# Performance work log

Hardware: AMD Instinct MI355X
Metric: run time of the kernel (lower is better)

Reference implementation:

```python
import jax, jax.numpy as jnp
import numpy as np

D_H, D_G, D_PROJ = 1280, 768, 256
SCALE = D_PROJ ** (-0.5)

def setup_inputs() -> dict:
    key = jax.random.key(0)
    k1, k2, k3, k4 = jax.random.split(key, 4)
    B, L, T = 8, 4096, 512
    H = jax.random.normal(k1, (B, L, D_H), dtype=jnp.float32)
    G = jax.random.normal(k2, (B, T, D_G), dtype=jnp.float32)
    attn_mask = jnp.zeros((B, L), dtype=bool)  # True = pad/ignore
    # nn.Linear weights: (out_features, in_features)
    Wk = jax.random.normal(k3, (D_PROJ, D_H), dtype=jnp.float32) * (D_H ** -0.5)
    Wq = jax.random.normal(k4, (D_PROJ, D_G), dtype=jnp.float32) * (D_G ** -0.5)
    return {"H": H, "G": G, "attn_mask": attn_mask, "Wk": Wk, "Wq": Wq}

def reference(H, G, attn_mask, Wk, Wq):
    # K = Wk(H): (B,L,P); Q = Wq(G): (B,T,P)
    K = jnp.einsum('bld,pd->blp', H, Wk)
    Q = jnp.einsum('btd,pd->btp', G, Wq)
    # scores (B,T,L); streaming two-pass softmax in the original is exactly
    # softmax over L -> compute it stably in one fused expression here.
    logits = jnp.einsum('btp,blp->btl', Q, K) * SCALE
    logits = jnp.where(attn_mask[:, None, :], -jnp.inf, logits)
    alpha = jax.nn.softmax(logits, axis=-1)
    Z = jnp.einsum('btl,bld->btd', alpha, H)  # (B,T,Dh)
    return Z
```

## Files before the change

kernel.cpp:

```cpp
#include <hip/hip_runtime.h>
#include <hip/hip_bf16.h>
#include <stdint.h>


typedef float f32x4 __attribute__((ext_vector_type(4)));
typedef short bf16x8 __attribute__((ext_vector_type(8)));

__device__ __forceinline__ unsigned short f2bf(float f) {
    __hip_bfloat16 h = __float2bfloat16(f);
    return __builtin_bit_cast(unsigned short, h);
}
__device__ __forceinline__ float bf2f(unsigned short h) {
    union { uint32_t u; float f; } v; v.u = ((uint32_t)h) << 16;
    return v.f;
}

__device__ __forceinline__ int xcdswz(int bx, int nbx) {
    int cpx = nbx >> 3;
    return (bx & 7) * cpx + (bx >> 3);
}

__device__ __forceinline__ void gload16(const unsigned short* g, unsigned short* l) {
    __builtin_amdgcn_global_load_lds(
        (const __attribute__((address_space(1))) void*)g,
        (__attribute__((address_space(3))) void*)l,
        16, 0, 0);
}

__device__ __forceinline__ int lidx(int row, int kshort) {
    return row * 40 + (((kshort >> 3) ^ ((row >> 3) & 3)) << 3) + (kshort & 7);
}

__global__ __launch_bounds__(256)
void cvt_f32_bf16(const float* __restrict__ in, unsigned short* __restrict__ out, long n4)
{
    long i = (long)blockIdx.x * 256 + threadIdx.x;
    if (i >= n4) return;
    float4 v = ((const float4*)in)[i];
    ushort4 w;
    w.x = f2bf(v.x); w.y = f2bf(v.y); w.z = f2bf(v.z); w.w = f2bf(v.w);
    ((ushort4*)out)[i] = w;
}

template<bool WRITE_HB>
__global__ __launch_bounds__(256)
void cvt_h(const float* __restrict__ H, unsigned short* __restrict__ Hbt,
           unsigned short* __restrict__ Hb)
{
    __shared__ unsigned short lT[64 * 72];
    const int ntile = 64 * 20 * 8;
    for (int tileid = blockIdx.x; tileid < ntile; tileid += gridDim.x) {
        int tmp = tileid;
        const int dt = tmp % 20; tmp /= 20;
        const int lt = tmp % 64;
        const int b  = tmp / 64;
        const int l0 = lt * 64, d0 = dt * 64;
        const float* Hs = H + ((long)b * 4096 + l0) * 1280 + d0;
        #pragma unroll
        for (int it = 0; it < 4; ++it) {
            int chunk = it * 256 + threadIdx.x;
            int lr = chunk >> 4, dc4 = (chunk & 15) << 2;
            float4 v = *(const float4*)(Hs + (long)lr * 1280 + dc4);
            unsigned short w[4] = { f2bf(v.x), f2bf(v.y), f2bf(v.z), f2bf(v.w) };
            if constexpr (WRITE_HB) {
                ushort4 wb = { w[0], w[1], w[2], w[3] };
                *(ushort4*)(Hb + ((long)b * 4096 + l0 + lr) * 1280 + d0 + dc4) = wb;
            }
            #pragma unroll
            for (int j = 0; j < 4; ++j) {
                int d = dc4 + j;
                int sl = (lr & 15) | ((((lr >> 4) ^ (d >> 2)) & 3) << 4);
                lT[d * 72 + sl] = w[j];
            }
        }
        __syncthreads();
        {
            int drow = threadIdx.x >> 2, lc = threadIdx.x & 3;
            int slc = lc ^ ((drow >> 2) & 3);
            const uint4* src = (const uint4*)(lT + drow * 72 + slc * 16);
            unsigned short* dst = Hbt + ((long)b * 1280 + d0 + drow) * 4096 + l0 + lc * 16;
            uint4 v0 = src[0], v1 = src[1];
            *(uint4*)(dst)     = v0;
            *(uint4*)(dst + 8) = v1;
        }
        __syncthreads();
    }
}

__global__ __launch_bounds__(256)
void gemm_proj(const float* __restrict__ Ap, const float* __restrict__ Bp,
               unsigned short* __restrict__ Cp, int M, int N, int K)
{
    __shared__ __align__(16) unsigned short lA[128 * 40];
    __shared__ __align__(16) unsigned short lB[128 * 40];

    const int bx = xcdswz(blockIdx.x, gridDim.x);
    const int nt = N >> 7;
    const int tm = bx / nt;
    const int tn = bx % nt;
    const int tid = threadIdx.x;
    const int lane = tid & 63, wv = tid >> 6;
    const int wr = wv >> 1, wc = wv & 1;
    const int fr = lane & 15, fk = lane >> 4;

    f32x4 acc[4][4] = {};

    for (int k0 = 0; k0 < K; k0 += 32) {
        {
            const float* A = Ap + (long)tm * 128 * K + k0;
            #pragma unroll
            for (int it = 0; it < 4; ++it) {
                int chunk = it * 256 + tid;
                int row = chunk >> 3;
                int kc  = (chunk & 7) << 2;
                const float4 v = *(const float4*)(A + (long)row * K + kc);
                ushort4 w;
                w.x = f2bf(v.x); w.y = f2bf(v.y); w.z = f2bf(v.z); w.w = f2bf(v.w);
                *(ushort4*)(&lA[lidx(row, kc)]) = w;
            }
        }
        {
            const float* B = Bp + (long)tn * 128 * K + k0;
            #pragma unroll
            for (int it = 0; it < 4; ++it) {
                int chunk = it * 256 + tid;
                int row = chunk >> 3;
                int kc  = (chunk & 7) << 2;
                const float4 v = *(const float4*)(B + (long)row * K + kc);
                ushort4 w;
                w.x = f2bf(v.x); w.y = f2bf(v.y); w.z = f2bf(v.z); w.w = f2bf(v.w);
                *(ushort4*)(&lB[lidx(row, kc)]) = w;
            }
        }
        __syncthreads();
        bf16x8 af[4], bfr[4];
        #pragma unroll
        for (int i = 0; i < 4; ++i)
            af[i] = *(const bf16x8*)(&lA[lidx(wr * 64 + i * 16 + fr, fk * 8)]);
        #pragma unroll
        for (int i = 0; i < 4; ++i)
            bfr[i] = *(const bf16x8*)(&lB[lidx(wc * 64 + i * 16 + fr, fk * 8)]);
        #pragma unroll
        for (int mi = 0; mi < 4; ++mi)
            #pragma unroll
            for (int ni = 0; ni < 4; ++ni)
                acc[mi][ni] = __builtin_amdgcn_mfma_f32_16x16x32_bf16(af[mi], bfr[ni], acc[mi][ni], 0, 0, 0);
        __syncthreads();
    }

    unsigned short* C = Cp + ((long)tm * 128) * N + (long)tn * 128;
    #pragma unroll
    for (int mi = 0; mi < 4; ++mi)
        #pragma unroll
        for (int ni = 0; ni < 4; ++ni)
            #pragma unroll
            for (int j = 0; j < 4; ++j) {
                int m = wr * 64 + mi * 16 + fk * 4 + j;
                int n = wc * 64 + ni * 16 + fr;
                C[(long)m * N + n] = f2bf(acc[mi][ni][j]);
            }
}

template<bool OF32>
__global__ __launch_bounds__(256)
void gemm_bt16s(const unsigned short* __restrict__ Ap, const unsigned short* __restrict__ Bp,
                void* __restrict__ Cp, int M, int N, int K,
                long sA, long sB, long sC, float scale)
{
    __shared__ __align__(16) unsigned short lA[128 * 64];
    __shared__ __align__(16) unsigned short lB[128 * 64];

    const int bx = xcdswz(blockIdx.x, gridDim.x);
    const int nt = N >> 7;
    const int tm = bx / nt, tn = bx % nt;
    const int b  = blockIdx.y;
    const int tid = threadIdx.x;
    const int lane = tid & 63, wv = tid >> 6;
    const int wr = wv >> 1, wc = wv & 1;
    const int fr = lane & 15, fk = lane >> 4;

    f32x4 acc[4][4] = {};

    const unsigned short* A0 = Ap + (long)b * sA + (long)tm * 128 * K;
    const unsigned short* B0 = Bp + (long)b * sB + (long)tn * 128 * K;

    for (int k0 = 0; k0 < K; k0 += 64) {
        #pragma unroll
        for (int q = 0; q < 4; ++q) {
            int slot = wv * 256 + q * 64 + lane;
            int row = slot >> 3, c = slot & 7;
            int ks = (c ^ (row & 7)) << 3;
            gload16(A0 + (long)row * K + k0 + ks, lA + (size_t)(wv * 256 + q * 64) * 8);
            gload16(B0 + (long)row * K + k0 + ks, lB + (size_t)(wv * 256 + q * 64) * 8);
        }
        __syncthreads();
        bf16x8 af[2][4], bfv[2][4];
        #pragma unroll
        for (int ks = 0; ks < 2; ++ks) {
            int csw = ((ks * 4 + fk) ^ (fr & 7)) << 3;
            #pragma unroll
            for (int i = 0; i < 4; ++i) {
                af[ks][i]  = *(const bf16x8*)(lA + (wr * 64 + i * 16 + fr) * 64 + csw);
                bfv[ks][i] = *(const bf16x8*)(lB + (wc * 64 + i * 16 + fr) * 64 + csw);
            }
        }
        #pragma unroll
        for (int mi = 0; mi < 4; ++mi)
            #pragma unroll
            for (int ni = 0; ni < 4; ++ni)
                #pragma unroll
                for (int ks = 0; ks < 2; ++ks)
                    acc[mi][ni] = __builtin_amdgcn_mfma_f32_16x16x32_bf16(af[ks][mi], bfv[ks][ni], acc[mi][ni], 0, 0, 0);
        __syncthreads();
    }

    if constexpr (OF32) {
        float* C = (float*)Cp + (long)b * sC + ((long)tm * 128) * N + (long)tn * 128;
        #pragma unroll
        for (int mi = 0; mi < 4; ++mi)
            #pragma unroll
            for (int ni = 0; ni < 4; ++ni)
                #pragma unroll
                for (int j = 0; j < 4; ++j) {
                    int m = wr * 64 + mi * 16 + fk * 4 + j;
                    int n = wc * 64 + ni * 16 + fr;
                    C[(long)m * N + n] = acc[mi][ni][j] * scale;
                }
    } else {
        unsigned short* C = (unsigned short*)Cp + (long)b * sC + ((long)tm * 128) * N + (long)tn * 128;
        #pragma unroll
        for (int mi = 0; mi < 4; ++mi)
            #pragma unroll
            for (int ni = 0; ni < 4; ++ni)
                #pragma unroll
                for (int j = 0; j < 4; ++j) {
                    int m = wr * 64 + mi * 16 + fk * 4 + j;
                    int n = wc * 64 + ni * 16 + fr;
                    C[(long)m * N + n] = f2bf(acc[mi][ni][j] * scale);
                }
    }
}

__global__ __launch_bounds__(256)
void gemm_kn(const unsigned short* __restrict__ Ap, const float* __restrict__ Bp,
             float* __restrict__ Cp, int M, int N, int K,
             long sA, long sB, long sC)
{
    __shared__ __align__(16) unsigned short lA[128 * 40];
    __shared__ __align__(16) unsigned short lB[64 * 40];

    const int bx = xcdswz(blockIdx.x, gridDim.x);
    const int mt = M >> 7;
    const int tm = bx % mt;
    const int tn = bx / mt;
    const int b  = blockIdx.y;
    const int tid = threadIdx.x;
    const int lane = tid & 63, wv = tid >> 6;
    const int wr = wv >> 1, wc = wv & 1;
    const int fr = lane & 15, fk = lane >> 4;

    f32x4 acc[4][2] = {};

    const unsigned short* A0 = Ap + (long)b * sA + (long)tm * 128 * K;
    const int nn    = tid & 63;
    const int khalf = tid >> 6;

    for (int k0 = 0; k0 < K; k0 += 32) {
        #pragma unroll
        for (int it = 0; it < 2; ++it) {
            int chunk = it * 256 + tid;
            int row = chunk >> 2;
            int kc  = (chunk & 3) << 3;
            *(uint4*)(&lA[lidx(row, kc)]) = *(const uint4*)(A0 + (long)row * K + k0 + kc);
        }
        {
            const float* Bb = Bp + (long)b * sB + (long)(k0 + khalf * 8) * N + (long)tn * 64 + nn;
            unsigned short t8[8];
            #pragma unroll
            for (int kk = 0; kk < 8; ++kk)
                t8[kk] = f2bf(Bb[(long)kk * N]);
            *(uint4*)(&lB[lidx(nn, khalf * 8)]) = *(uint4*)(&t8[0]);
        }
        __syncthreads();
        bf16x8 af[4], bfr[2];
        #pragma unroll
        for (int i = 0; i < 4; ++i)
            af[i] = *(const bf16x8*)(&lA[lidx(wr * 64 + i * 16 + fr, fk * 8)]);
        #pragma unroll
        for (int i = 0; i < 2; ++i)
            bfr[i] = *(const bf16x8*)(&lB[lidx(wc * 32 + i * 16 + fr, fk * 8)]);
        #pragma unroll
        for (int mi = 0; mi < 4; ++mi)
            #pragma unroll
            for (int ni = 0; ni < 2; ++ni)
                acc[mi][ni] = __builtin_amdgcn_mfma_f32_16x16x32_bf16(af[mi], bfr[ni], acc[mi][ni], 0, 0, 0);
        __syncthreads();
    }

    float* C = Cp + (long)b * sC + ((long)tm * 128) * N + (long)tn * 64;
    #pragma unroll
    for (int mi = 0; mi < 4; ++mi)
        #pragma unroll
        for (int ni = 0; ni < 2; ++ni)
            #pragma unroll
            for (int j = 0; j < 4; ++j) {
                int m = wr * 64 + mi * 16 + fk * 4 + j;
                int n = wc * 32 + ni * 16 + fr;
                C[(long)m * N + n] = acc[mi][ni][j];
            }
}

__global__ __launch_bounds__(256)
void softmax_rows(unsigned short* __restrict__ S, const unsigned char* __restrict__ mask)
{
    const int row = blockIdx.x;
    const int b = row >> 9;
    const long base = (long)row * 4096;
    const int tid = threadIdx.x, lane = tid & 63, wv = tid >> 6;
    __shared__ float red[8];

    uint4 s0 = *(const uint4*)(S + base + tid * 16);
    uint4 s1 = *(const uint4*)(S + base + tid * 16 + 8);
    uint4 mv = *(const uint4*)(mask + (long)b * 4096 + tid * 16);
    const unsigned char* mb = (const unsigned char*)&mv;

    unsigned int words[8] = { s0.x, s0.y, s0.z, s0.w, s1.x, s1.y, s1.z, s1.w };
    float x[16];
    #pragma unroll
    for (int i = 0; i < 8; ++i) {
        x[2 * i]     = bf2f((unsigned short)(words[i] & 0xffffu));
        x[2 * i + 1] = bf2f((unsigned short)(words[i] >> 16));
    }
    #pragma unroll
    for (int i = 0; i < 16; ++i)
        if (mb[i]) x[i] = -1e30f;

    float m = x[0];
    #pragma unroll
    for (int i = 1; i < 16; ++i) m = fmaxf(m, x[i]);
    #pragma unroll
    for (int off = 32; off; off >>= 1) m = fmaxf(m, __shfl_xor(m, off));
    if (lane == 0) red[wv] = m;
    __syncthreads();
    m = fmaxf(fmaxf(red[0], red[1]), fmaxf(red[2], red[3]));

    float p[16];
    float s = 0.f;
    #pragma unroll
    for (int i = 0; i < 16; ++i) { p[i] = __expf(x[i] - m); s += p[i]; }
    #pragma unroll
    for (int off = 32; off; off >>= 1) s += __shfl_xor(s, off);
    if (lane == 0) red[4 + wv] = s;
    __syncthreads();
    s = (red[4] + red[5]) + (red[6] + red[7]);
    const float inv = 1.0f / s;

    unsigned int ow[8];
    #pragma unroll
    for (int i = 0; i < 8; ++i) {
        unsigned int lo = f2bf(p[2 * i] * inv);
        unsigned int hi = f2bf(p[2 * i + 1] * inv);
        ow[i] = lo | (hi << 16);
    }
    uint4 o0 = { ow[0], ow[1], ow[2], ow[3] };
    uint4 o1 = { ow[4], ow[5], ow[6], ow[7] };
    *(uint4*)(S + base + tid * 16)     = o0;
    *(uint4*)(S + base + tid * 16 + 8) = o1;
}

extern "C" void kernel_launch(void* const* d_in, const int* in_sizes, int n_in,
                              void* d_out, int out_size, void* d_ws, size_t ws_size,
                              hipStream_t stream)
{
    const float*         H    = (const float*)d_in[0];
    const float*         G    = (const float*)d_in[1];
    const unsigned char* mask = (const unsigned char*)d_in[2];
    const float*         Wk   = (const float*)d_in[3];
    const float*         Wq   = (const float*)d_in[4];
    float*               out  = (float*)d_out;

    const long nK = (long)8 * 4096 * 256;
    const long nQ = (long)8 * 512 * 256;
    const long nS = (long)8 * 512 * 4096;
    const long nH = (long)8 * 1280 * 4096;
    const long nW = (long)256 * 1280;

    unsigned short* Kb  = (unsigned short*)d_ws;
    unsigned short* Qb  = Kb + nK;
    unsigned short* Sb  = Qb + nQ;
    unsigned short* Hbt = Sb + nS;
    unsigned short* Hb  = Hbt + nH;
    unsigned short* Wkb = Hb + nH;

    const size_t need2 = (size_t)(nK + nQ + nS + nH + nH + nW) * 2;
    const size_t need1 = (size_t)(nK + nQ + nS + nH) * 2;

    if (ws_size >= need2) {
        cvt_f32_bf16<<<dim3(320), 256, 0, stream>>>(Wk, Wkb, nW / 4);
        cvt_h<true><<<dim3(2048), 256, 0, stream>>>(H, Hbt, Hb);
        gemm_bt16s<false><<<dim3(512, 1), 256, 0, stream>>>(
            Hb, Wkb, Kb, 32768, 256, 1280, 0, 0, 0, 1.0f);
        gemm_proj<<<dim3(64, 1), 256, 0, stream>>>(G, Wq, Qb, 4096, 256, 768);
        gemm_bt16s<false><<<dim3(128, 8), 256, 0, stream>>>(
            Qb, Kb, Sb, 512, 4096, 256,
            (long)512 * 256, (long)4096 * 256, (long)512 * 4096, 0.0625f);
        softmax_rows<<<dim3(4096), 256, 0, stream>>>(Sb, mask);
        gemm_bt16s<true><<<dim3(40, 8), 256, 0, stream>>>(
            Sb, Hbt, out, 512, 1280, 4096,
            (long)512 * 4096, (long)1280 * 4096, (long)512 * 1280, 1.0f);
    } else if (ws_size >= need1) {
        gemm_proj<<<dim3(512, 1), 256, 0, stream>>>(H, Wk, Kb, 32768, 256, 1280);
        gemm_proj<<<dim3(64, 1), 256, 0, stream>>>(G, Wq, Qb, 4096, 256, 768);
        cvt_h<false><<<dim3(2048), 256, 0, stream>>>(H, Hbt, nullptr);
        gemm_bt16s<false><<<dim3(128, 8), 256, 0, stream>>>(
            Qb, Kb, Sb, 512, 4096, 256,
            (long)512 * 256, (long)4096 * 256, (long)512 * 4096, 0.0625f);
        softmax_rows<<<dim3(4096), 256, 0, stream>>>(Sb, mask);
        gemm_bt16s<true><<<dim3(40, 8), 256, 0, stream>>>(
            Sb, Hbt, out, 512, 1280, 4096,
            (long)512 * 4096, (long)1280 * 4096, (long)512 * 1280, 1.0f);
    } else {
        gemm_proj<<<dim3(512, 1), 256, 0, stream>>>(H, Wk, Kb, 32768, 256, 1280);
        gemm_proj<<<dim3(64, 1), 256, 0, stream>>>(G, Wq, Qb, 4096, 256, 768);
        gemm_bt16s<false><<<dim3(128, 8), 256, 0, stream>>>(
            Qb, Kb, Sb, 512, 4096, 256,
            (long)512 * 256, (long)4096 * 256, (long)512 * 4096, 0.0625f);
        softmax_rows<<<dim3(4096), 256, 0, stream>>>(Sb, mask);
        gemm_kn<<<dim3(80, 8), 256, 0, stream>>>(
            Sb, H, out, 512, 1280, 4096,
            (long)512 * 4096, (long)4096 * 1280, (long)512 * 1280);
    }
}
```

Measured before the change: 271.7 us.

## Split-K the alpha·H GEMM into four slices with a separate reduction kernel

Replaces the final 40x8-block GEMM (Z = alpha·H) with a split-K version that launches 160x8 blocks, each covering a quarter of the 4096-long reduction. Partial fp32 results go into workspace reused from the Hb buffer, and a small kernel then sums the four slices into the output. The aim is to fill the GPU, since 320 blocks underuse the CUs on this part. In exchange it writes and re-reads four fp32 partial Z tensors and adds one more launch. The new GEMM also uses a 64-wide K step with XOR-swizzled LDS and no double buffering.

New measurement: 275.5 us. No clear change (+1.4%).

```diff
diff --git a/kernel.cpp b/kernel.cpp
--- a/kernel.cpp
+++ b/kernel.cpp
@@ -242,6 +242,87 @@
 }
 
 __global__ __launch_bounds__(256)
+void zsplit(const unsigned short* __restrict__ Sb, const unsigned short* __restrict__ Hbt,
+            float* __restrict__ Zp)
+{
+    __shared__ __align__(16) unsigned short lA[128 * 64];
+    __shared__ __align__(16) unsigned short lB[128 * 64];
+
+    const int K = 4096, N = 1280, KS = 1024;
+    const long nZ = (long)8 * 512 * 1280;
+
+    const int bx = xcdswz(blockIdx.x, gridDim.x);
+    const int tm = bx & 3;
+    const int tn = (bx >> 2) % 10;
+    const int ks = bx / 40;
+    const int b  = blockIdx.y;
+    const int tid = threadIdx.x;
+    const int lane = tid & 63, wv = tid >> 6;
+    const int wr = wv >> 1, wc = wv & 1;
+    const int fr = lane & 15, fk = lane >> 4;
+
+    f32x4 acc[4][4] = {};
+
+    const unsigned short* A0 = Sb  + ((long)b * 512  + tm * 128) * K + ks * KS;
+    const unsigned short* B0 = Hbt + ((long)b * 1280 + tn * 128) * K + ks * KS;
+
+    for (int k0 = 0; k0 < KS; k0 += 64) {
+        #pragma unroll
+        for (int q = 0; q < 4; ++q) {
+            int slot = wv * 256 + q * 64 + lane;
+            int row = slot >> 3, c = slot & 7;
+            int kc = (c ^ (row & 7)) << 3;
+            gload16(A0 + (long)row * K + k0 + kc, lA + (size_t)(wv * 256 + q * 64) * 8);
+            gload16(B0 + (long)row * K + k0 + kc, lB + (size_t)(wv * 256 + q * 64) * 8);
+        }
+        __syncthreads();
+        bf16x8 af[2][4], bfv[2][4];
+        #pragma unroll
+        for (int kk = 0; kk < 2; ++kk) {
+            int csw = ((kk * 4 + fk) ^ (fr & 7)) << 3;
+            #pragma unroll
+            for (int i = 0; i < 4; ++i) {
+                af[kk][i]  = *(const bf16x8*)(lA + (wr * 64 + i * 16 + fr) * 64 + csw);
+                bfv[kk][i] = *(const bf16x8*)(lB + (wc * 64 + i * 16 + fr) * 64 + csw);
+            }
+        }
+        #pragma unroll
+        for (int mi = 0; mi < 4; ++mi)
+            #pragma unroll
+            for (int ni = 0; ni < 4; ++ni)
+                #pragma unroll
+                for (int kk = 0; kk < 2; ++kk)
+                    acc[mi][ni] = __builtin_amdgcn_mfma_f32_16x16x32_bf16(af[kk][mi], bfv[kk][ni], acc[mi][ni], 0, 0, 0);
+        __syncthreads();
+    }
+
+    float* C = Zp + (long)ks * nZ + ((long)b * 512 + tm * 128) * N + tn * 128;
+    #pragma unroll
+    for (int mi = 0; mi < 4; ++mi)
+        #pragma unroll
+        for (int ni = 0; ni < 4; ++ni)
+            #pragma unroll
+            for (int j = 0; j < 4; ++j) {
+                int m = wr * 64 + mi * 16 + fk * 4 + j;
+                int n = wc * 64 + ni * 16 + fr;
+                C[(long)m * N + n] = acc[mi][ni][j];
+            }
+}
+
+__global__ __launch_bounds__(256)
+void reduce4(const float* __restrict__ p, float* __restrict__ out, long n4)
+{
+    long i = (long)blockIdx.x * 256 + threadIdx.x;
+    if (i >= n4) return;
+    const long s = n4;
+    f32x4 a = ((const f32x4*)p)[i];
+    f32x4 b = ((const f32x4*)p)[i + s];
+    f32x4 c = ((const f32x4*)p)[i + 2 * s];
+    f32x4 d = ((const f32x4*)p)[i + 3 * s];
+    ((f32x4*)out)[i] = (a + b) + (c + d);
+}
+
+__global__ __launch_bounds__(256)
 void gemm_kn(const unsigned short* __restrict__ Ap, const float* __restrict__ Bp,
              float* __restrict__ Cp, int M, int N, int K,
              long sA, long sB, long sC)
@@ -384,6 +465,7 @@
     const long nS = (long)8 * 512 * 4096;
     const long nH = (long)8 * 1280 * 4096;
     const long nW = (long)256 * 1280;
+    const long nZ = (long)8 * 512 * 1280;
 
     unsigned short* Kb  = (unsigned short*)d_ws;
     unsigned short* Qb  = Kb + nK;
@@ -391,6 +473,7 @@
     unsigned short* Hbt = Sb + nS;
     unsigned short* Hb  = Hbt + nH;
     unsigned short* Wkb = Hb + nH;
+    float*          Zp  = (float*)Hb;
 
     const size_t need2 = (size_t)(nK + nQ + nS + nH + nH + nW) * 2;
     const size_t need1 = (size_t)(nK + nQ + nS + nH) * 2;
@@ -405,9 +488,8 @@
             Qb, Kb, Sb, 512, 4096, 256,
             (long)512 * 256, (long)4096 * 256, (long)512 * 4096, 0.0625f);
         softmax_rows<<<dim3(4096), 256, 0, stream>>>(Sb, mask);
-        gemm_bt16s<true><<<dim3(40, 8), 256, 0, stream>>>(
-            Sb, Hbt, out, 512, 1280, 4096,
-            (long)512 * 4096, (long)1280 * 4096, (long)512 * 1280, 1.0f);
+        zsplit<<<dim3(160, 8), 256, 0, stream>>>(Sb, Hbt, Zp);
+        reduce4<<<dim3(5120), 256, 0, stream>>>(Zp, out, nZ / 4);
     } else if (ws_size >= need1) {
         gemm_proj<<<dim3(512, 1), 256, 0, stream>>>(H, Wk, Kb, 32768, 256, 1280);
         gemm_proj<<<dim3(64, 1), 256, 0, stream>>>(G, Wq, Qb, 4096, 256, 768);
```
